# Optimization experiments

Hardware: AMD Instinct MI355X
Metric: run time of the kernel (lower is better)

## Reference

```python
import jax, jax.numpy as jnp
import numpy as np

B, S, D = 1, 2048, 1024
H, DH = 16, 64
FF_INNER = 4 * D          # 4096
FUSED = 2 * FF_INNER      # 8192
ROT_BASE = 1000.0


def _rope_tables(seq_len, dim_head):
    # rotarizer: inv_freq = (base ** (arange(0, dh, 2)/dh)) ** -1 ; cached in bfloat16
    inv_freq = 1.0 / (ROT_BASE ** (jnp.arange(0, dim_head, 2, dtype=jnp.float32) / dim_head))
    t = jnp.arange(seq_len, dtype=jnp.float32)
    freqs = jnp.outer(t, inv_freq)                     # [S, DH/2]
    cos = jnp.cos(freqs).astype(jnp.bfloat16)[None, :, None, :]  # [1,S,1,DH/2]
    sin = jnp.sin(freqs).astype(jnp.bfloat16)[None, :, None, :]
    return cos, sin


def _apply_rope(x, cos, sin):
    d = x.shape[-1] // 2
    x1, x2 = x[..., :d], x[..., d:]
    y1 = x1 * cos + x2 * sin
    y2 = -x1 * sin + x2 * cos
    return jnp.concatenate([y1, y2], axis=-1).astype(x.dtype)


def _l2norm(x):
    # F.normalize(p=2, dim=-1), eps=1e-12
    n = jnp.linalg.norm(x, axis=-1, keepdims=True)
    return x / jnp.maximum(n, 1e-12)


def setup_inputs() -> dict:
    key = jax.random.key(0)
    ks = jax.random.split(key, 12)
    std = 0.02
    inp = {
        "h_states": jax.random.normal(ks[0], (B, S, D), jnp.float32),
        "Wq": jax.random.normal(ks[1], (D, D), jnp.float32) * std,
        "Wk": jax.random.normal(ks[2], (D, D), jnp.float32) * std,
        "Wv": jax.random.normal(ks[3], (D, D), jnp.float32) * std,
        "Wqb": jax.random.normal(ks[4], (D, D), jnp.float32) * std,
        "Wkb": jax.random.normal(ks[5], (D, D), jnp.float32) * std,
        "Wo": jax.random.normal(ks[6], (D, D), jnp.float32) * std,
        "bo": jnp.zeros((D,), jnp.float32),
        "W1": jax.random.normal(ks[7], (D, FUSED), jnp.float32) * std,
        "b1": jnp.zeros((FUSED,), jnp.float32),
        "W2": jax.random.normal(ks[8], (FF_INNER, D), jnp.float32) * std,
        "b2": jnp.zeros((D,), jnp.float32),
        "learnedlambda": jnp.asarray(1.0, jnp.float32),
        # l2normscale init: log(S^2 - S) for training_seqlen S
        "l2normscale": jnp.asarray(np.log(float(S) ** 2 - float(S)), np.float32),
    }
    return inp


def reference(h_states, Wq, Wk, Wv, Wqb, Wkb, Wo, bo, W1, b1, W2, b2, learnedlambda, l2normscale):
    b, s, d = h_states.shape
    scale = DH ** -0.5

    # layerwisenorm: RMSNorm, no affine
    eps = jnp.finfo(h_states.dtype).eps
    x = h_states * jax.lax.rsqrt(jnp.mean(jnp.square(h_states), axis=-1, keepdims=True) + eps)

    # projections -> [B,S,H,DH]
    def proj(W):
        return (x @ W).reshape(b, s, H, DH)
    q, k, v = proj(Wq), proj(Wk), proj(Wv)
    qb, kb = proj(Wqb), proj(Wkb)

    cos, sin = _rope_tables(s, DH)
    # per-head qk-norm (l2norm) then rope; v untouched
    q = _apply_rope(_l2norm(q), cos, sin)
    k = _apply_rope(_l2norm(k), cos, sin)
    qb = _apply_rope(_l2norm(qb), cos, sin)
    kb = _apply_rope(_l2norm(kb), cos, sin)

    causal = jnp.tril(jnp.ones((s, s), bool))  # [S,S]

    # main attention: scale=1 (l2norm path), causal softmax, scaled by l2normscale
    scores = jnp.einsum("bqhd,bkhd->bhqk", q, k)
    scores = jnp.where(causal[None, None], scores, -jnp.inf)
    attn = jax.nn.softmax(scores, axis=-1)
    y = l2normscale * jnp.einsum("bhqk,bkhd->bhqd", attn, v)  # [B,H,S,DH]

    # bias attention: masked raw scores @ ones == causal row-sum, broadcast over DH
    sb = jnp.einsum("bqhd,bkhd->bhqk", qb, kb) * scale
    sb = jnp.where(causal[None, None], sb, 0.0)
    y = y + jnp.sum(sb, axis=-1, keepdims=True)  # broadcast over head dim

    y = y.transpose(0, 2, 1, 3).reshape(b, s, d)
    attn_out = y @ Wo + bo

    # fused SwiGLU: chunk -> (x_part, gate); silu(gate) * x_part
    u = x @ W1 + b1
    xp, gate = u[..., :FF_INNER], u[..., FF_INNER:]
    ff = (jax.nn.silu(gate) * xp) @ W2 + b2

    return h_states * learnedlambda + ff + attn_out
```

## Files before the change

### kernel.cpp

```cpp
#include <hip/hip_runtime.h>
#include <hip/hip_bf16.h>
#include <math.h>

typedef __bf16 bf16x8 __attribute__((ext_vector_type(8)));
typedef float  f32x4  __attribute__((ext_vector_type(4)));

#define GLD16(g, l) __builtin_amdgcn_global_load_lds(                      \
    (const __attribute__((address_space(1))) void*)(g),                    \
    (__attribute__((address_space(3))) void*)(l), 16, 0, 0)

#define SCHED_FENCE() __builtin_amdgcn_sched_barrier(0)


__device__ __forceinline__ void tconv_tile(const float* __restrict__ in,
                                           __bf16* __restrict__ out,
                                           int ldin, int ldout,
                                           int r0, int c0, int tid) {
  __shared__ float t[32][33];
  int tx = tid & 31, ty = tid >> 5;
  #pragma unroll
  for (int i = ty; i < 32; i += 8)
    t[i][tx] = in[(size_t)(r0 + i) * ldin + c0 + tx];
  __syncthreads();
  #pragma unroll
  for (int i = ty; i < 32; i += 8)
    out[(size_t)(c0 + i) * ldout + r0 + tx] = (__bf16)t[tx][i];
}

__global__ __launch_bounds__(256) void tconv_k(const float* __restrict__ in,
                                               __bf16* __restrict__ out,
                                               int ldin, int ldout) {
  tconv_tile(in, out, ldin, ldout, blockIdx.y * 32, blockIdx.x * 32, threadIdx.x);
}

__global__ __launch_bounds__(256) void tconvw1p_k(const float* __restrict__ W1,
                                                  __bf16* __restrict__ out) {
  int c0 = blockIdx.x * 32;
  int src_c0 = ((c0 >> 5) & 1) * 4096 + (c0 >> 6) * 32;
  __shared__ float t[32][33];
  int r0 = blockIdx.y * 32;
  int tid = threadIdx.x, tx = tid & 31, ty = tid >> 5;
  #pragma unroll
  for (int i = ty; i < 32; i += 8)
    t[i][tx] = W1[(size_t)(r0 + i) * 8192 + src_c0 + tx];
  __syncthreads();
  #pragma unroll
  for (int i = ty; i < 32; i += 8)
    out[(size_t)(c0 + i) * 1024 + r0 + tx] = (__bf16)t[tx][i];
}

__global__ __launch_bounds__(256) void tconv5_k(const float* __restrict__ w0,
    const float* __restrict__ w1, const float* __restrict__ w2,
    const float* __restrict__ w3, const float* __restrict__ w4,
    __bf16* __restrict__ out) {
  const float* src[5] = {w0, w1, w2, w3, w4};
  int z = blockIdx.z;
  tconv_tile(src[z], out + (size_t)z * 1048576, 1024, 1024,
             blockIdx.y * 32, blockIdx.x * 32, threadIdx.x);
}

__global__ __launch_bounds__(256) void tconvwow2_k(const float* __restrict__ Wo,
    const float* __restrict__ W2, __bf16* __restrict__ WoW2t) {
  int tid = threadIdx.x;
  if (blockIdx.z == 0) {
    if (blockIdx.y >= 32) return;
    __shared__ float t[32][33];
    int r0 = blockIdx.y * 32, c0 = blockIdx.x * 32;
    int tx = tid & 31, ty = tid >> 5;
    #pragma unroll
    for (int i = ty; i < 32; i += 8)
      t[i][tx] = Wo[(size_t)(r0 + i) * 1024 + c0 + tx];
    __syncthreads();
    #pragma unroll
    for (int i = ty; i < 32; i += 8)
      WoW2t[(size_t)(c0 + i) * 5120 + r0 + tx] = (__bf16)t[tx][i];
  } else {
    __shared__ float t[32][33];
    int r0 = blockIdx.y * 32, c0 = blockIdx.x * 32;
    int tx = tid & 31, ty = tid >> 5;
    #pragma unroll
    for (int i = ty; i < 32; i += 8)
      t[i][tx] = W2[(size_t)(r0 + i) * 1024 + c0 + tx];
    __syncthreads();
    #pragma unroll
    for (int i = ty; i < 32; i += 8)
      WoW2t[(size_t)(c0 + i) * 5120 + 1024 + r0 + tx] = (__bf16)t[tx][i];
  }
}

__global__ __launch_bounds__(256) void rmsnorm_k(const float* __restrict__ hs,
                                                 __bf16* __restrict__ x) {
  int row = blockIdx.x, tid = threadIdx.x;
  const float4 v = ((const float4*)(hs + (size_t)row * 1024))[tid];
  float ss = v.x * v.x + v.y * v.y + v.z * v.z + v.w * v.w;
  #pragma unroll
  for (int o = 32; o > 0; o >>= 1) ss += __shfl_xor(ss, o);
  __shared__ float ps[4];
  if ((tid & 63) == 0) ps[tid >> 6] = ss;
  __syncthreads();
  float tot = ps[0] + ps[1] + ps[2] + ps[3];
  float r = rsqrtf(tot * (1.0f / 1024.0f) + 1.1920929e-7f);
  __bf16* xr = x + (size_t)row * 1024 + tid * 4;
  xr[0] = (__bf16)(v.x * r); xr[1] = (__bf16)(v.y * r);
  xr[2] = (__bf16)(v.z * r); xr[3] = (__bf16)(v.w * r);
}

__global__ __launch_bounds__(256, 3) void gemm_bt_k(
    const __bf16* __restrict__ A, const __bf16* __restrict__ Bt,
    float* __restrict__ C, int N, int K) {
  __shared__ __bf16 sA[3][128 * 32];
  __shared__ __bf16 sB[3][128 * 32];
  const int tid = threadIdx.x;
  const int lane = tid & 63;
  const int quad = lane >> 4, l16 = lane & 15;
  const int wave = tid >> 6;
  const int waveM = wave >> 1, waveN = wave & 1;
  const int m0 = blockIdx.y * 128, n0 = blockIdx.x * 128;
  const int nk = K >> 5;
  const int rowS = tid >> 2;
  const int kg = ((tid & 3) ^ ((rowS >> 1) & 3)) * 8;
  const __bf16* gA0 = A + (size_t)(m0 + rowS) * K + kg;
  const __bf16* gA1 = gA0 + (size_t)64 * K;
  const __bf16* gB0 = Bt + (size_t)(n0 + rowS) * K + kg;
  const __bf16* gB1 = gB0 + (size_t)64 * K;
  const int lo0 = tid * 8, lo1 = 2048 + tid * 8;

  auto stage = [&](int t) {
    int s = t % 3;
    __bf16* dA = sA[s];
    __bf16* dB = sB[s];
    GLD16(gA0 + t * 32, dA + lo0);
    GLD16(gA1 + t * 32, dA + lo1);
    GLD16(gB0 + t * 32, dB + lo0);
    GLD16(gB1 + t * 32, dB + lo1);
  };
  stage(0); stage(1);

  f32x4 acc[4][4] = {};
  #pragma unroll 1
  for (int i = 0; i < nk; ++i) {
    if (i < nk - 1)
      asm volatile("s_waitcnt vmcnt(4)" ::: "memory");
    else
      asm volatile("s_waitcnt vmcnt(0)" ::: "memory");
    __builtin_amdgcn_s_barrier();
    SCHED_FENCE();
    int cs = i % 3;
    const __bf16* cA = sA[cs];
    const __bf16* cB = sB[cs];
    if (i + 2 < nk) stage(i + 2);
    SCHED_FENCE();
    bf16x8 af[4], bfv[4];
    #pragma unroll
    for (int mt = 0; mt < 4; ++mt) {
      int r = waveM * 64 + mt * 16 + l16;
      af[mt] = *(const bf16x8*)(cA + r * 32 + ((quad ^ ((r >> 1) & 3)) * 8));
    }
    #pragma unroll
    for (int nt = 0; nt < 4; ++nt) {
      int r = waveN * 64 + nt * 16 + l16;
      bfv[nt] = *(const bf16x8*)(cB + r * 32 + ((quad ^ ((r >> 1) & 3)) * 8));
    }
    __builtin_amdgcn_s_setprio(1);
    #pragma unroll
    for (int mt = 0; mt < 4; ++mt)
      #pragma unroll
      for (int nt = 0; nt < 4; ++nt)
        acc[mt][nt] = __builtin_amdgcn_mfma_f32_16x16x32_bf16(af[mt], bfv[nt], acc[mt][nt], 0, 0, 0);
    __builtin_amdgcn_s_setprio(0);
    SCHED_FENCE();
  }
  #pragma unroll
  for (int mt = 0; mt < 4; ++mt) {
    int row = m0 + waveM * 64 + mt * 16 + quad * 4;
    #pragma unroll
    for (int nt = 0; nt < 4; ++nt) {
      int col = n0 + waveN * 64 + nt * 16 + l16;
      #pragma unroll
      for (int r = 0; r < 4; ++r)
        C[(size_t)(row + r) * N + col] = acc[mt][nt][r];
    }
  }
}

__global__ __launch_bounds__(256, 3) void gemm_partk_k(
    const __bf16* __restrict__ A, const __bf16* __restrict__ Bt,
    float* __restrict__ P, int N, int K) {
  __shared__ __bf16 sA[3][128 * 32];
  __shared__ __bf16 sB[3][128 * 32];
  const int tid = threadIdx.x;
  const int lane = tid & 63;
  const int quad = lane >> 4, l16 = lane & 15;
  const int wave = tid >> 6;
  const int waveM = wave >> 1, waveN = wave & 1;
  const int m0 = blockIdx.y * 128, n0 = blockIdx.x * 128;
  const int kz = blockIdx.z, nz = gridDim.z;
  const int kper = K / nz, kbeg = kz * kper;
  const int nk = kper >> 5;
  const size_t MN = (size_t)gridDim.y * 128 * N;
  float* C = P + (size_t)kz * MN;
  const int rowS = tid >> 2;
  const int kg = ((tid & 3) ^ ((rowS >> 1) & 3)) * 8;
  const __bf16* gA0 = A + (size_t)(m0 + rowS) * K + kbeg + kg;
  const __bf16* gA1 = gA0 + (size_t)64 * K;
  const __bf16* gB0 = Bt + (size_t)(n0 + rowS) * K + kbeg + kg;
  const __bf16* gB1 = gB0 + (size_t)64 * K;
  const int lo0 = tid * 8, lo1 = 2048 + tid * 8;

  auto stage = [&](int t) {
    int s = t % 3;
    __bf16* dA = sA[s];
    __bf16* dB = sB[s];
    GLD16(gA0 + t * 32, dA + lo0);
    GLD16(gA1 + t * 32, dA + lo1);
    GLD16(gB0 + t * 32, dB + lo0);
    GLD16(gB1 + t * 32, dB + lo1);
  };
  stage(0); stage(1);

  f32x4 acc[4][4] = {};
  #pragma unroll 1
  for (int i = 0; i < nk; ++i) {
    if (i < nk - 1)
      asm volatile("s_waitcnt vmcnt(4)" ::: "memory");
    else
      asm volatile("s_waitcnt vmcnt(0)" ::: "memory");
    __builtin_amdgcn_s_barrier();
    SCHED_FENCE();
    int cs = i % 3;
    const __bf16* cA = sA[cs];
    const __bf16* cB = sB[cs];
    if (i + 2 < nk) stage(i + 2);
    SCHED_FENCE();
    bf16x8 af[4], bfv[4];
    #pragma unroll
    for (int mt = 0; mt < 4; ++mt) {
      int r = waveM * 64 + mt * 16 + l16;
      af[mt] = *(const bf16x8*)(cA + r * 32 + ((quad ^ ((r >> 1) & 3)) * 8));
    }
    #pragma unroll
    for (int nt = 0; nt < 4; ++nt) {
      int r = waveN * 64 + nt * 16 + l16;
      bfv[nt] = *(const bf16x8*)(cB + r * 32 + ((quad ^ ((r >> 1) & 3)) * 8));
    }
    __builtin_amdgcn_s_setprio(1);
    #pragma unroll
    for (int mt = 0; mt < 4; ++mt)
      #pragma unroll
      for (int nt = 0; nt < 4; ++nt)
        acc[mt][nt] = __builtin_amdgcn_mfma_f32_16x16x32_bf16(af[mt], bfv[nt], acc[mt][nt], 0, 0, 0);
    __builtin_amdgcn_s_setprio(0);
    SCHED_FENCE();
  }
  #pragma unroll
  for (int mt = 0; mt < 4; ++mt) {
    int row = m0 + waveM * 64 + mt * 16 + quad * 4;
    #pragma unroll
    for (int nt = 0; nt < 4; ++nt) {
      int col = n0 + waveN * 64 + nt * 16 + l16;
      #pragma unroll
      for (int r = 0; r < 4; ++r)
        C[(size_t)(row + r) * N + col] = acc[mt][nt][r];
    }
  }
}

__global__ __launch_bounds__(512, 2) void ffn1silu_k(
    const __bf16* __restrict__ A, const __bf16* __restrict__ W1t,
    const float* __restrict__ b1, __bf16* __restrict__ ffout) {
  __shared__ __bf16 sA[4][256 * 32];
  __shared__ __bf16 sB[4][256 * 32];
  const int tid = threadIdx.x, lane = tid & 63, w = tid >> 6;
  const int quad = lane >> 4, l16 = lane & 15;
  const int wm = w >> 2, wn = w & 3;
  const int m0 = blockIdx.y * 256;
  const int n0p = blockIdx.x * 256;
  const int K = 1024, NKT = 32;
  const int rowS = tid >> 2;
  const int kg = ((tid & 3) ^ ((rowS >> 1) & 3)) * 8;
  const __bf16* gA0 = A + (size_t)(m0 + rowS) * K + kg;
  const __bf16* gA1 = gA0 + (size_t)128 * K;
  const __bf16* gB0 = W1t + (size_t)(n0p + rowS) * K + kg;
  const __bf16* gB1 = gB0 + (size_t)128 * K;
  const int lo0 = tid * 8, lo1 = 4096 + tid * 8;

  f32x4 acc[8][4] = {};

  auto stageA = [&](int t) {
    __bf16* d = sA[t & 3];
    GLD16(gA0 + t * 32, d + lo0);
    GLD16(gA1 + t * 32, d + lo1);
  };
  auto stageB = [&](int t) {
    __bf16* d = sB[t & 3];
    GLD16(gB0 + t * 32, d + lo0);
    GLD16(gB1 + t * 32, d + lo1);
  };

  auto compute_half = [&](const __bf16* cA, const bf16x8* bfr, int half) {
    bf16x8 af[4];
    #pragma unroll
    for (int mt = 0; mt < 4; ++mt) {
      int r = wm * 128 + half * 64 + mt * 16 + l16;
      af[mt] = *(const bf16x8*)(cA + r * 32 + ((quad ^ ((r >> 1) & 3)) * 8));
    }
    __builtin_amdgcn_s_setprio(1);
    #pragma unroll
    for (int mt = 0; mt < 4; ++mt)
      #pragma unroll
      for (int nt = 0; nt < 4; ++nt)
        acc[half * 4 + mt][nt] = __builtin_amdgcn_mfma_f32_16x16x32_bf16(
            af[mt], bfr[nt], acc[half * 4 + mt][nt], 0, 0, 0);
    __builtin_amdgcn_s_setprio(0);
  };

  stageA(0); stageB(0);
  stageA(1); stageB(1);
  stageA(2); stageB(2);

  #pragma unroll 1
  for (int t = 0; t < NKT; ++t) {
    if (t < NKT - 2)
      asm volatile("s_waitcnt vmcnt(8)" ::: "memory");
    else if (t == NKT - 2)
      asm volatile("s_waitcnt vmcnt(4)" ::: "memory");
    else
      asm volatile("s_waitcnt vmcnt(0)" ::: "memory");
    __builtin_amdgcn_s_barrier();
    SCHED_FENCE();
    const __bf16* cA = sA[t & 3];
    const __bf16* cB = sB[t & 3];
    if (t + 3 < NKT) stageA(t + 3);
    SCHED_FENCE();
    bf16x8 bfr[4];
    #pragma unroll
    for (int nt = 0; nt < 4; ++nt) {
      int r = wn * 64 + nt * 16 + l16;
      bfr[nt] = *(const bf16x8*)(cB + r * 32 + ((quad ^ ((r >> 1) & 3)) * 8));
    }
    compute_half(cA, bfr, 0);
    SCHED_FENCE();
    if (t + 3 < NKT) stageB(t + 3);
    SCHED_FENCE();
    compute_half(cA, bfr, 1);
    SCHED_FENCE();
  }

  const int colbase = (blockIdx.x * 4 + wn) * 32;
  #pragma unroll
  for (int j = 0; j < 8; ++j) {
    int row = m0 + wm * 128 + (j >> 2) * 64 + (j & 3) * 16 + quad * 4;
    #pragma unroll
    for (int p = 0; p < 2; ++p) {
      int col = colbase + p * 16 + l16;
      float bxv = b1[col], bgv = b1[col + 4096];
      #pragma unroll
      for (int r = 0; r < 4; ++r) {
        float xp = acc[j][p][r] + bxv;
        float g  = acc[j][p + 2][r] + bgv;
        float val = xp * g / (1.f + __expf(-g));
        ffout[(size_t)(row + r) * 5120 + 1024 + col] = (__bf16)val;
      }
    }
  }
}

__global__ __launch_bounds__(256) void combine_k(
    const float* __restrict__ P, const float* __restrict__ b2,
    const float* __restrict__ bo, const float* __restrict__ hs,
    const float* __restrict__ plam, float* __restrict__ out) {
  const size_t MN = (size_t)2048 * 1024;
  size_t i = ((size_t)blockIdx.x * 256 + threadIdx.x) * 4;
  int col = (int)(i & 1023);
  float4 a0 = *(const float4*)(P + i);
  float4 a1 = *(const float4*)(P + MN + i);
  float4 a2 = *(const float4*)(P + 2 * MN + i);
  float4 a3 = *(const float4*)(P + 3 * MN + i);
  float4 h  = *(const float4*)(hs + i);
  float4 v2 = *(const float4*)(b2 + col);
  float4 vo = *(const float4*)(bo + col);
  float lam = plam[0];
  float4 o;
  o.x = (a0.x + a1.x) + (a2.x + a3.x) + v2.x + vo.x + lam * h.x;
  o.y = (a0.y + a1.y) + (a2.y + a3.y) + v2.y + vo.y + lam * h.y;
  o.z = (a0.z + a1.z) + (a2.z + a3.z) + v2.z + vo.z + lam * h.z;
  o.w = (a0.w + a1.w) + (a2.w + a3.w) + v2.w + vo.w + lam * h.w;
  *(float4*)(out + i) = o;
}

__global__ __launch_bounds__(256) void qkprep_k(const float* __restrict__ proj,
    __bf16* __restrict__ qo, __bf16* __restrict__ ko,
    float* __restrict__ qbo, float* __restrict__ kbo) {
  int gw = blockIdx.x * 4 + (threadIdx.x >> 6);
  int lane = threadIdx.x & 63;
  int s = gw >> 4, h = gw & 15;
  int j = lane & 31;
  float inv = powf(1000.0f, -(float)j * (1.0f / 32.0f));
  float ang = (float)s * inv;
  float cb = (float)(__bf16)cosf(ang);
  float sb = (float)(__bf16)sinf(ang);
  size_t ibase = (size_t)s * 5120 + h * 64 + lane;
  size_t obase = (size_t)s * 1024 + h * 64 + lane;
  bool lo = lane < 32;

  auto proc = [&](const float* src) -> float {
    float xv = src[ibase];
    float ss = xv * xv;
    #pragma unroll
    for (int o = 32; o > 0; o >>= 1) ss += __shfl_xor(ss, o);
    float y = xv / fmaxf(sqrtf(ss), 1e-12f);
    float yp = __shfl_xor(y, 32);
    return lo ? (y * cb + yp * sb) : (y * cb - yp * sb);
  };
  qo[obase]  = (__bf16)proc(proj + 0);
  ko[obase]  = (__bf16)proc(proj + 1024);
  qbo[obase] = proc(proj + 3072);
  kbo[obase] = proc(proj + 4096);
}

__global__ __launch_bounds__(64) void kbsum_k(const float* __restrict__ kb,
                                              float* __restrict__ tsum) {
  int t = blockIdx.x, h = blockIdx.y, d = threadIdx.x;
  size_t base = (size_t)h * 64 + d;
  float s = 0.f;
  #pragma unroll 4
  for (int r = 0; r < 32; ++r)
    s += kb[(size_t)(t * 32 + r) * 1024 + base];
  tsum[(t * 16 + h) * 64 + d] = s;
}

__global__ __launch_bounds__(64) void sbrow2_k(const float* __restrict__ qb,
                                               const float* __restrict__ kb,
                                               const float* __restrict__ tsum,
                                               float* __restrict__ sb) {
  int t = blockIdx.x, h = blockIdx.y, d = threadIdx.x;
  size_t base = (size_t)h * 64 + d;
  float run = 0.f;
  for (int tp = 0; tp < t; ++tp) run += tsum[(tp * 16 + h) * 64 + d];
  for (int s0 = 0; s0 < 32; s0 += 4) {
    float p[4];
    #pragma unroll
    for (int u = 0; u < 4; ++u) {
      size_t off = (size_t)(t * 32 + s0 + u) * 1024 + base;
      run += kb[off];
      p[u] = qb[off] * run;
    }
    #pragma unroll
    for (int o = 32; o > 0; o >>= 1) {
      #pragma unroll
      for (int u = 0; u < 4; ++u) p[u] += __shfl_xor(p[u], o);
    }
    if (d == 0) {
      #pragma unroll
      for (int u = 0; u < 4; ++u) sb[(t * 32 + s0 + u) * 16 + h] = 0.125f * p[u];
    }
  }
}

__global__ __launch_bounds__(256) void attn_k(const __bf16* __restrict__ qg,
    const __bf16* __restrict__ kg, const __bf16* __restrict__ vtg,
    float* __restrict__ o_part, float* __restrict__ m_part,
    float* __restrict__ l_part) {
  __shared__ __bf16 sK[64 * 64];
  __shared__ __bf16 sVt[64 * 64];
  __shared__ __bf16 sP[4][16 * 64];
  const int pair = blockIdx.x, j4 = blockIdx.y, hh = blockIdx.z;
  const int tid = threadIdx.x, lane = tid & 63, w = tid >> 6;
  const int quad = lane >> 4, l16 = lane & 15;
  const int srow = tid >> 3;
  const int sg = (tid & 7) ^ (srow & 7);
  __bf16* ldsK = sK + tid * 8;
  __bf16* ldsV = sVt + tid * 8;
  __bf16* sPw = sP[w];

  for (int phase = 0; phase < 2; ++phase) {
    const int qt = phase ? 31 - pair : pair;
    const int q0 = qt * 64;
    const int n = qt + 1;
    const int kb = (j4 * n) >> 2, ke = ((j4 + 1) * n) >> 2;
    bf16x8 qf[2];
    #pragma unroll
    for (int kk = 0; kk < 2; ++kk)
      qf[kk] = *(const bf16x8*)(qg + (size_t)(q0 + w * 16 + l16) * 1024 + hh * 64 + kk * 32 + quad * 8);
    f32x4 accO[4] = {};
    float m_[4], l_[4];
    #pragma unroll
    for (int r = 0; r < 4; ++r) { m_[r] = -INFINITY; l_[r] = 0.f; }

    for (int kt = kb; kt < ke; ++kt) {
      const __bf16* gK = kg + (size_t)(kt * 64 + srow) * 1024 + hh * 64 + sg * 8;
      const __bf16* gV = vtg + (size_t)(hh * 64 + srow) * 2048 + kt * 64 + sg * 8;
      GLD16(gK, ldsK);
      GLD16(gK + (size_t)32 * 1024, ldsK + 2048);
      GLD16(gV, ldsV);
      GLD16(gV + (size_t)32 * 2048, ldsV + 2048);
      __syncthreads();

      f32x4 s4[4];
      #pragma unroll
      for (int nt = 0; nt < 4; ++nt) {
        int r = nt * 16 + l16;
        bf16x8 b0 = *(const bf16x8*)(sK + r * 64 + ((quad ^ (r & 7)) * 8));
        bf16x8 b1 = *(const bf16x8*)(sK + r * 64 + (((4 + quad) ^ (r & 7)) * 8));
        f32x4 sa = {0.f, 0.f, 0.f, 0.f};
        sa = __builtin_amdgcn_mfma_f32_16x16x32_bf16(qf[0], b0, sa, 0, 0, 0);
        sa = __builtin_amdgcn_mfma_f32_16x16x32_bf16(qf[1], b1, sa, 0, 0, 0);
        s4[nt] = sa;
      }
      if (kt == qt) {
        #pragma unroll
        for (int nt = 0; nt < 4; ++nt)
          #pragma unroll
          for (int r = 0; r < 4; ++r)
            if (nt * 16 + l16 > w * 16 + quad * 4 + r) s4[nt][r] = -INFINITY;
      }
      float mx[4], al[4], rs[4];
      #pragma unroll
      for (int r = 0; r < 4; ++r)
        mx[r] = fmaxf(fmaxf(s4[0][r], s4[1][r]), fmaxf(s4[2][r], s4[3][r]));
      #pragma unroll
      for (int o = 1; o < 16; o <<= 1)
        #pragma unroll
        for (int r = 0; r < 4; ++r) mx[r] = fmaxf(mx[r], __shfl_xor(mx[r], o));
      #pragma unroll
      for (int r = 0; r < 4; ++r) {
        float mn = fmaxf(m_[r], mx[r]);
        al[r] = __expf(m_[r] - mn);
        m_[r] = mn;
      }
      float p[4][4];
      #pragma unroll
      for (int nt = 0; nt < 4; ++nt)
        #pragma unroll
        for (int r = 0; r < 4; ++r)
          p[nt][r] = __expf(s4[nt][r] - m_[r]);
      #pragma unroll
      for (int r = 0; r < 4; ++r)
        rs[r] = (p[0][r] + p[1][r]) + (p[2][r] + p[3][r]);
      #pragma unroll
      for (int o = 1; o < 16; o <<= 1)
        #pragma unroll
        for (int r = 0; r < 4; ++r) rs[r] += __shfl_xor(rs[r], o);
      #pragma unroll
      for (int r = 0; r < 4; ++r) l_[r] = l_[r] * al[r] + rs[r];
      #pragma unroll
      for (int nt = 0; nt < 4; ++nt)
        #pragma unroll
        for (int r = 0; r < 4; ++r) accO[nt][r] *= al[r];
      #pragma unroll
      for (int nt = 0; nt < 4; ++nt)
        #pragma unroll
        for (int r = 0; r < 4; ++r) {
          int row = quad * 4 + r, col = nt * 16 + l16;
          sPw[row * 64 + (col ^ ((row & 7) << 3))] = (__bf16)p[nt][r];
        }
      #pragma unroll
      for (int kk = 0; kk < 2; ++kk) {
        bf16x8 a = *(const bf16x8*)(sPw + l16 * 64 + (((kk * 4 + quad) ^ (l16 & 7)) * 8));
        #pragma unroll
        for (int nt = 0; nt < 4; ++nt) {
          int vr = nt * 16 + l16;
          bf16x8 bv = *(const bf16x8*)(sVt + vr * 64 + (((kk * 4 + quad) ^ (vr & 7)) * 8));
          accO[nt] = __builtin_amdgcn_mfma_f32_16x16x32_bf16(a, bv, accO[nt], 0, 0, 0);
        }
      }
      __syncthreads();
    }
    #pragma unroll
    for (int r = 0; r < 4; ++r) {
      int grow = q0 + w * 16 + quad * 4 + r;
      if (l16 == 0) {
        m_part[((size_t)j4 * 2048 + grow) * 16 + hh] = m_[r];
        l_part[((size_t)j4 * 2048 + grow) * 16 + hh] = l_[r];
      }
      #pragma unroll
      for (int nt = 0; nt < 4; ++nt)
        o_part[((size_t)j4 * 2048 + grow) * 1024 + hh * 64 + nt * 16 + l16] = accO[nt][r];
    }
  }
}

__global__ __launch_bounds__(256) void attnmerge_k(const float* __restrict__ o_part,
    const float* __restrict__ m_part, const float* __restrict__ l_part,
    const float* __restrict__ sbr, const float* __restrict__ pl2s,
    __bf16* __restrict__ yo) {
  int idx = blockIdx.x * 256 + threadIdx.x;
  int s = idx >> 8, rem = idx & 255;
  int h = rem >> 4, dg = (rem & 15) * 4;
  float m[4], l[4];
  #pragma unroll
  for (int j = 0; j < 4; ++j) {
    m[j] = m_part[((size_t)j * 2048 + s) * 16 + h];
    l[j] = l_part[((size_t)j * 2048 + s) * 16 + h];
  }
  float M = fmaxf(fmaxf(m[0], m[1]), fmaxf(m[2], m[3]));
  float den = 0.f;
  float4 acc = {0.f, 0.f, 0.f, 0.f};
  #pragma unroll
  for (int j = 0; j < 4; ++j) {
    float e = __expf(m[j] - M);
    den += l[j] * e;
    float4 o = *(const float4*)(o_part + ((size_t)j * 2048 + s) * 1024 + h * 64 + dg);
    acc.x += e * o.x; acc.y += e * o.y; acc.z += e * o.z; acc.w += e * o.w;
  }
  float sc = pl2s[0] / den;
  float add = sbr[s * 16 + h];
  __bf16* yp = yo + (size_t)s * 5120 + h * 64 + dg;
  yp[0] = (__bf16)(sc * acc.x + add);
  yp[1] = (__bf16)(sc * acc.y + add);
  yp[2] = (__bf16)(sc * acc.z + add);
  yp[3] = (__bf16)(sc * acc.w + add);
}

extern "C" void kernel_launch(void* const* d_in, const int* in_sizes, int n_in,
                              void* d_out, int out_size, void* d_ws, size_t ws_size,
                              hipStream_t stream) {
  (void)in_sizes; (void)n_in; (void)out_size; (void)ws_size;
  const float* hs   = (const float*)d_in[0];
  const float* Wq   = (const float*)d_in[1];
  const float* Wk   = (const float*)d_in[2];
  const float* Wv   = (const float*)d_in[3];
  const float* Wqb  = (const float*)d_in[4];
  const float* Wkb  = (const float*)d_in[5];
  const float* Wo   = (const float*)d_in[6];
  const float* bo   = (const float*)d_in[7];
  const float* W1   = (const float*)d_in[8];
  const float* b1   = (const float*)d_in[9];
  const float* W2   = (const float*)d_in[10];
  const float* b2   = (const float*)d_in[11];
  const float* plam = (const float*)d_in[12];
  const float* pl2s = (const float*)d_in[13];
  float* out = (float*)d_out;
  char* ws = (char*)d_ws;

  size_t off = 0;
  auto alloc = [&](size_t bytes) { char* p = ws + off; off += (bytes + 255) & ~(size_t)255; return p; };
  __bf16* Wt5    = (__bf16*)alloc((size_t)5 * 1024 * 1024 * 2);
  __bf16* WoW2t  = (__bf16*)alloc((size_t)1024 * 5120 * 2);
  __bf16* W1t    = (__bf16*)alloc((size_t)8192 * 1024 * 2);
  __bf16* xbf    = (__bf16*)alloc((size_t)2048 * 1024 * 2);
  __bf16* concat = (__bf16*)alloc((size_t)2048 * 5120 * 2);
  float*  proj  = (float*)alloc((size_t)2048 * 5120 * 4);
  float*  qbf32 = (float*)alloc((size_t)2048 * 1024 * 4);
  float*  kbf32 = (float*)alloc((size_t)2048 * 1024 * 4);
  __bf16* qbf   = (__bf16*)alloc((size_t)2048 * 1024 * 2);
  __bf16* kbf   = (__bf16*)alloc((size_t)2048 * 1024 * 2);
  float*  o_part = proj;
  float*  m_part = qbf32;
  float*  l_part = qbf32 + (size_t)4 * 2048 * 16;
  float*  gpart  = proj;
  __bf16* vtbf  = (__bf16*)alloc((size_t)1024 * 2048 * 2);
  float*  sbrow = (float*)alloc((size_t)2048 * 16 * 4);
  float*  tsum  = (float*)alloc((size_t)64 * 16 * 64 * 4);

  tconv5_k<<<dim3(32, 32, 5), 256, 0, stream>>>(Wq, Wk, Wv, Wqb, Wkb, Wt5);
  tconvwow2_k<<<dim3(32, 128, 2), 256, 0, stream>>>(Wo, W2, WoW2t);
  tconvw1p_k<<<dim3(256, 32), 256, 0, stream>>>(W1, W1t);

  rmsnorm_k<<<2048, 256, 0, stream>>>(hs, xbf);
  gemm_bt_k<<<dim3(40, 16), 256, 0, stream>>>(xbf, Wt5, proj, 5120, 1024);
  qkprep_k<<<8192, 256, 0, stream>>>(proj, qbf, kbf, qbf32, kbf32);
  tconv_k<<<dim3(32, 64), 256, 0, stream>>>(proj + 2048, vtbf, 5120, 2048);
  kbsum_k<<<dim3(64, 16), 64, 0, stream>>>(kbf32, tsum);
  sbrow2_k<<<dim3(64, 16), 64, 0, stream>>>(qbf32, kbf32, tsum, sbrow);
  attn_k<<<dim3(16, 4, 16), 256, 0, stream>>>(qbf, kbf, vtbf, o_part, m_part, l_part);
  attnmerge_k<<<2048, 256, 0, stream>>>(o_part, m_part, l_part, sbrow, pl2s, concat);
  ffn1silu_k<<<dim3(32, 8), 512, 0, stream>>>(xbf, W1t, b1, concat);
  gemm_partk_k<<<dim3(8, 16, 4), 256, 0, stream>>>(concat, WoW2t, gpart, 1024, 5120);
  combine_k<<<2048, 256, 0, stream>>>(gpart, b2, bo, hs, plam, out);
}
```

Baseline: 372.5 us.

## Double-buffer K/V tiles in attention and widen bias-sum kernels to four waves

The attention kernel now keeps two LDS buffers for K and V^T and issues the async global-to-LDS loads for the next key tile before computing on the current one. This overlaps memory latency with MFMA work and drops one barrier per iteration. The kb row-sum and bias-row kernels now use 256 threads, with each wave taking 8 rows and writing extra per-wave partial sums (tsum8), which gives them more parallelism. RoPE table generation also switches to exp2f and fast __sinf/__cosf intrinsics, which may slightly change bf16-rounded values for large angles.

```diff
diff --git a/kernel.cpp b/kernel.cpp
--- a/kernel.cpp
+++ b/kernel.cpp
@@ -395,10 +395,10 @@
   int lane = threadIdx.x & 63;
   int s = gw >> 4, h = gw & 15;
   int j = lane & 31;
-  float inv = powf(1000.0f, -(float)j * (1.0f / 32.0f));
+  float inv = exp2f(-0.31143076f * (float)j);
   float ang = (float)s * inv;
-  float cb = (float)(__bf16)cosf(ang);
-  float sb = (float)(__bf16)sinf(ang);
+  float cb = (float)(__bf16)__cosf(ang);
+  float sb = (float)(__bf16)__sinf(ang);
   size_t ibase = (size_t)s * 5120 + h * 64 + lane;
   size_t obase = (size_t)s * 1024 + h * 64 + lane;
   bool lo = lane < 32;
@@ -418,30 +418,41 @@
   kbo[obase] = proc(proj + 4096);
 }
 
-__global__ __launch_bounds__(64) void kbsum_k(const float* __restrict__ kb,
-                                              float* __restrict__ tsum) {
-  int t = blockIdx.x, h = blockIdx.y, d = threadIdx.x;
+__global__ __launch_bounds__(256) void kbsum_k(const float* __restrict__ kb,
+                                               float* __restrict__ tsum,
+                                               float* __restrict__ tsum8) {
+  int t = blockIdx.x, h = blockIdx.y;
+  int d = threadIdx.x & 63, w = threadIdx.x >> 6;
   size_t base = (size_t)h * 64 + d;
   float s = 0.f;
-  #pragma unroll 4
-  for (int r = 0; r < 32; ++r)
-    s += kb[(size_t)(t * 32 + r) * 1024 + base];
-  tsum[(t * 16 + h) * 64 + d] = s;
-}
-
-__global__ __launch_bounds__(64) void sbrow2_k(const float* __restrict__ qb,
-                                               const float* __restrict__ kb,
-                                               const float* __restrict__ tsum,
-                                               float* __restrict__ sb) {
-  int t = blockIdx.x, h = blockIdx.y, d = threadIdx.x;
+  #pragma unroll
+  for (int r = 0; r < 8; ++r)
+    s += kb[(size_t)(t * 32 + w * 8 + r) * 1024 + base];
+  tsum8[(size_t)((t * 4 + w) * 16 + h) * 64 + d] = s;
+  __shared__ float ps[4][64];
+  ps[w][d] = s;
+  __syncthreads();
+  if (w == 0)
+    tsum[(size_t)(t * 16 + h) * 64 + d] = (ps[0][d] + ps[1][d]) + (ps[2][d] + ps[3][d]);
+}
+
+__global__ __launch_bounds__(256) void sbrow2_k(const float* __restrict__ qb,
+                                                const float* __restrict__ kb,
+                                                const float* __restrict__ tsum,
+                                                const float* __restrict__ tsum8,
+                                                float* __restrict__ sb) {
+  int t = blockIdx.x, h = blockIdx.y;
+  int d = threadIdx.x & 63, g = threadIdx.x >> 6;
   size_t base = (size_t)h * 64 + d;
   float run = 0.f;
-  for (int tp = 0; tp < t; ++tp) run += tsum[(tp * 16 + h) * 64 + d];
-  for (int s0 = 0; s0 < 32; s0 += 4) {
+  for (int tp = 0; tp < t; ++tp) run += tsum[(size_t)(tp * 16 + h) * 64 + d];
+  for (int w = 0; w < g; ++w) run += tsum8[(size_t)((t * 4 + w) * 16 + h) * 64 + d];
+  int r0 = t * 32 + g * 8;
+  for (int s0 = 0; s0 < 8; s0 += 4) {
     float p[4];
     #pragma unroll
     for (int u = 0; u < 4; ++u) {
-      size_t off = (size_t)(t * 32 + s0 + u) * 1024 + base;
+      size_t off = (size_t)(r0 + s0 + u) * 1024 + base;
       run += kb[off];
       p[u] = qb[off] * run;
     }
@@ -452,7 +463,7 @@
     }
     if (d == 0) {
       #pragma unroll
-      for (int u = 0; u < 4; ++u) sb[(t * 32 + s0 + u) * 16 + h] = 0.125f * p[u];
+      for (int u = 0; u < 4; ++u) sb[(r0 + s0 + u) * 16 + h] = 0.125f * p[u];
     }
   }
 }
@@ -461,17 +472,25 @@
     const __bf16* __restrict__ kg, const __bf16* __restrict__ vtg,
     float* __restrict__ o_part, float* __restrict__ m_part,
     float* __restrict__ l_part) {
-  __shared__ __bf16 sK[64 * 64];
-  __shared__ __bf16 sVt[64 * 64];
+  __shared__ __bf16 sK[2][64 * 64];
+  __shared__ __bf16 sVt[2][64 * 64];
   __shared__ __bf16 sP[4][16 * 64];
   const int pair = blockIdx.x, j4 = blockIdx.y, hh = blockIdx.z;
   const int tid = threadIdx.x, lane = tid & 63, w = tid >> 6;
   const int quad = lane >> 4, l16 = lane & 15;
   const int srow = tid >> 3;
   const int sg = (tid & 7) ^ (srow & 7);
-  __bf16* ldsK = sK + tid * 8;
-  __bf16* ldsV = sVt + tid * 8;
   __bf16* sPw = sP[w];
+
+  auto stage = [&](int kt) {
+    int b = kt & 1;
+    const __bf16* gK = kg + (size_t)(kt * 64 + srow) * 1024 + hh * 64 + sg * 8;
+    const __bf16* gV = vtg + (size_t)(hh * 64 + srow) * 2048 + kt * 64 + sg * 8;
+    GLD16(gK, sK[b] + tid * 8);
+    GLD16(gK + (size_t)32 * 1024, sK[b] + tid * 8 + 2048);
+    GLD16(gV, sVt[b] + tid * 8);
+    GLD16(gV + (size_t)32 * 2048, sVt[b] + tid * 8 + 2048);
+  };
 
   for (int phase = 0; phase < 2; ++phase) {
     const int qt = phase ? 31 - pair : pair;
@@ -487,21 +506,23 @@
     #pragma unroll
     for (int r = 0; r < 4; ++r) { m_[r] = -INFINITY; l_[r] = 0.f; }
 
+    __syncthreads();
+    if (kb < ke) stage(kb);
+
     for (int kt = kb; kt < ke; ++kt) {
-      const __bf16* gK = kg + (size_t)(kt * 64 + srow) * 1024 + hh * 64 + sg * 8;
-      const __bf16* gV = vtg + (size_t)(hh * 64 + srow) * 2048 + kt * 64 + sg * 8;
-      GLD16(gK, ldsK);
-      GLD16(gK + (size_t)32 * 1024, ldsK + 2048);
-      GLD16(gV, ldsV);
-      GLD16(gV + (size_t)32 * 2048, ldsV + 2048);
       __syncthreads();
+      SCHED_FENCE();
+      if (kt + 1 < ke) stage(kt + 1);
+      SCHED_FENCE();
+      const __bf16* cK = sK[kt & 1];
+      const __bf16* cV = sVt[kt & 1];
 
       f32x4 s4[4];
       #pragma unroll
       for (int nt = 0; nt < 4; ++nt) {
         int r = nt * 16 + l16;
-        bf16x8 b0 = *(const bf16x8*)(sK + r * 64 + ((quad ^ (r & 7)) * 8));
-        bf16x8 b1 = *(const bf16x8*)(sK + r * 64 + (((4 + quad) ^ (r & 7)) * 8));
+        bf16x8 b0 = *(const bf16x8*)(cK + r * 64 + ((quad ^ (r & 7)) * 8));
+        bf16x8 b1 = *(const bf16x8*)(cK + r * 64 + (((4 + quad) ^ (r & 7)) * 8));
         f32x4 sa = {0.f, 0.f, 0.f, 0.f};
         sa = __builtin_amdgcn_mfma_f32_16x16x32_bf16(qf[0], b0, sa, 0, 0, 0);
         sa = __builtin_amdgcn_mfma_f32_16x16x32_bf16(qf[1], b1, sa, 0, 0, 0);
@@ -560,11 +581,10 @@
         #pragma unroll
         for (int nt = 0; nt < 4; ++nt) {
           int vr = nt * 16 + l16;
-          bf16x8 bv = *(const bf16x8*)(sVt + vr * 64 + (((kk * 4 + quad) ^ (vr & 7)) * 8));
+          bf16x8 bv = *(const bf16x8*)(cV + vr * 64 + (((kk * 4 + quad) ^ (vr & 7)) * 8));
           accO[nt] = __builtin_amdgcn_mfma_f32_16x16x32_bf16(a, bv, accO[nt], 0, 0, 0);
         }
       }
-      __syncthreads();
     }
     #pragma unroll
     for (int r = 0; r < 4; ++r) {
@@ -652,6 +672,7 @@
   __bf16* vtbf  = (__bf16*)alloc((size_t)1024 * 2048 * 2);
   float*  sbrow = (float*)alloc((size_t)2048 * 16 * 4);
   float*  tsum  = (float*)alloc((size_t)64 * 16 * 64 * 4);
+  float*  tsum8 = (float*)alloc((size_t)256 * 16 * 64 * 4);
 
   tconv5_k<<<dim3(32, 32, 5), 256, 0, stream>>>(Wq, Wk, Wv, Wqb, Wkb, Wt5);
   tconvwow2_k<<<dim3(32, 128, 2), 256, 0, stream>>>(Wo, W2, WoW2t);
@@ -661,8 +682,8 @@
   gemm_bt_k<<<dim3(40, 16), 256, 0, stream>>>(xbf, Wt5, proj, 5120, 1024);
   qkprep_k<<<8192, 256, 0, stream>>>(proj, qbf, kbf, qbf32, kbf32);
   tconv_k<<<dim3(32, 64), 256, 0, stream>>>(proj + 2048, vtbf, 5120, 2048);
-  kbsum_k<<<dim3(64, 16), 64, 0, stream>>>(kbf32, tsum);
-  sbrow2_k<<<dim3(64, 16), 64, 0, stream>>>(qbf32, kbf32, tsum, sbrow);
+  kbsum_k<<<dim3(64, 16), 256, 0, stream>>>(kbf32, tsum, tsum8);
+  sbrow2_k<<<dim3(64, 16), 256, 0, stream>>>(qbf32, kbf32, tsum, tsum8, sbrow);
   attn_k<<<dim3(16, 4, 16), 256, 0, stream>>>(qbf, kbf, vtbf, o_part, m_part, l_part);
   attnmerge_k<<<2048, 256, 0, stream>>>(o_part, m_part, l_part, sbrow, pl2s, concat);
   ffn1silu_k<<<dim3(32, 8), 512, 0, stream>>>(xbf, W1t, b1, concat);
```

After: 361.2 us. -3.0%, faster.
